# Optimization experiments

Measured on AMD Instinct MI355X. Metric: run time of the kernel, lower is better.

Reference implementation:

```python
import jax, jax.numpy as jnp
import numpy as np

N_NODES = 100000
N_REL = 5
IN_F = 128
HID = 128

def _glorot(key, shape):
    fan_in, fan_out = shape[-2], shape[-1]
    s = jnp.sqrt(6.0 / (fan_in + fan_out))
    return jax.random.uniform(key, shape, jnp.float32, -s, s)

def setup_inputs() -> dict:
    key = jax.random.key(0)
    ks = jax.random.split(key, 16)
    x = jax.random.normal(ks[0], (N_NODES, IN_F), jnp.float32)
    edge_index = jax.random.randint(ks[1], (2, 1600000), 0, N_NODES, jnp.int32)
    edge_type = jax.random.randint(ks[2], (1600000,), 0, N_REL, jnp.int32)
    d = {"x": x, "edge_index": edge_index, "edge_type": edge_type}
    dims = [(IN_F, HID), (HID, HID), (HID, HID)]
    for li, (fi, fo) in enumerate(dims, start=1):
        d[f"W{li}"] = _glorot(ks[3 * li], (N_REL, fi, fo))        # per-relation weights
        d[f"root{li}"] = _glorot(ks[3 * li + 1], (fi, fo))        # root/self weight
        d[f"b{li}"] = jnp.zeros((fo,), jnp.float32)               # bias
    return d

def _rgcn_conv(x, src, dst, edge_type, W, root, b):
    # out = x @ root + b + sum_r segment_mean_r(x[src] @ W_r -> dst)
    out = x @ root + b
    for r in range(N_REL):  # small fixed relation count
        m = (edge_type == r).astype(x.dtype)                      # [E]
        h = (x @ W[r])[src] * m[:, None]                          # [E, out]
        s = jax.ops.segment_sum(h, dst, num_segments=N_NODES)     # [N, out]
        c = jax.ops.segment_sum(m, dst, num_segments=N_NODES)     # [N]
        out = out + s / jnp.maximum(c, 1.0)[:, None]
    return out

def reference(x, edge_index, edge_type, W1, root1, b1, W2, root2, b2, W3, root3, b3):
    src, dst = edge_index[0], edge_index[1]
    # dropout is identity in eval mode; applied as identity here
    h = jax.nn.relu(_rgcn_conv(x, src, dst, edge_type, W1, root1, b1))
    h = jax.nn.relu(_rgcn_conv(h, src, dst, edge_type, W2, root2, b2))
    h = jax.nn.relu(_rgcn_conv(h, src, dst, edge_type, W3, root3, b3))
    return h
```

## Files before the change

kernel.cpp:

```cpp
#include <hip/hip_runtime.h>

#define N_NODES_C 100000
#define N_REL_C 5
#define N_TOT (N_REL_C * N_NODES_C)
#define FEAT 128
#define KTOT 768
#define BM 128
#define GBK 64

typedef __attribute__((ext_vector_type(8))) short bf16x8;
typedef __attribute__((ext_vector_type(4))) float f32x4;

__device__ inline unsigned short f2bf(float f) {
    union { float f; unsigned int u; } v; v.f = f;
    return (unsigned short)((v.u + 0x7FFFu + ((v.u >> 16) & 1u)) >> 16);
}

__device__ __forceinline__ void g2l16(const void* g, void* l) {
    __builtin_amdgcn_global_load_lds((const __attribute__((address_space(1))) unsigned int*)g,
                                     (__attribute__((address_space(3))) unsigned int*)l,
                                     16, 0, 0);
}

__global__ __launch_bounds__(256) void count_edges(const int* __restrict__ dst,
                                                   const int* __restrict__ et,
                                                   int* __restrict__ cnt, int E) {
    int e = blockIdx.x * 256 + threadIdx.x;
    if (e < E) atomicAdd(&cnt[et[e] * N_NODES_C + dst[e]], 1);
}

__global__ __launch_bounds__(256) void make_inv(const int* __restrict__ cnt,
                                                float* __restrict__ inv, int n) {
    int i = blockIdx.x * 256 + threadIdx.x;
    if (i < n) inv[i] = 1.0f / (float)(cnt[i] > 1 ? cnt[i] : 1);
}

__global__ __launch_bounds__(256) void scan_block(const int* __restrict__ cnt,
                                                  int* __restrict__ rowptr,
                                                  int* __restrict__ bsum, int n) {
    __shared__ int sh[256];
    int tid = threadIdx.x;
    int i = blockIdx.x * 256 + tid;
    int v = (i < n) ? cnt[i] : 0;
    sh[tid] = v;
    __syncthreads();
#pragma unroll
    for (int o = 1; o < 256; o <<= 1) {
        int t = (tid >= o) ? sh[tid - o] : 0;
        __syncthreads();
        sh[tid] += t;
        __syncthreads();
    }
    if (i < n) rowptr[i] = sh[tid] - v;
    if (tid == 255) bsum[blockIdx.x] = sh[255];
}

__global__ __launch_bounds__(256) void scan_bsum(int* __restrict__ bsum, int nb) {
    __shared__ int sh[256];
    __shared__ int carry;
    int tid = threadIdx.x;
    if (tid == 0) carry = 0;
    __syncthreads();
    for (int base = 0; base < nb; base += 256) {
        int i = base + tid;
        int v = (i < nb) ? bsum[i] : 0;
        sh[tid] = v;
        __syncthreads();
#pragma unroll
        for (int o = 1; o < 256; o <<= 1) {
            int t = (tid >= o) ? sh[tid - o] : 0;
            __syncthreads();
            sh[tid] += t;
            __syncthreads();
        }
        int excl = sh[tid] - v + carry;
        int chunk_total = sh[255];
        __syncthreads();
        if (i < nb) bsum[i] = excl;
        if (tid == 0) carry += chunk_total;
        __syncthreads();
    }
}

__global__ __launch_bounds__(256) void scan_add(int* __restrict__ rowptr,
                                                const int* __restrict__ bsum,
                                                int n, int Etot) {
    int i = blockIdx.x * 256 + threadIdx.x;
    if (i < n) rowptr[i] += bsum[blockIdx.x];
    if (i == 0) rowptr[n] = Etot;
}

__global__ __launch_bounds__(256) void fill_csr(const int* __restrict__ src,
                                                const int* __restrict__ dst,
                                                const int* __restrict__ et,
                                                int* __restrict__ cursor,
                                                int* __restrict__ esrc, int E) {
    int e = blockIdx.x * 256 + threadIdx.x;
    if (e < E) {
        int pos = atomicAdd(&cursor[et[e] * N_NODES_C + dst[e]], 1);
        esrc[pos] = src[e];
    }
}

__global__ __launch_bounds__(256) void convert_x(const float* __restrict__ x,
                                                 unsigned short* __restrict__ xb, int n4) {
    int i = blockIdx.x * 256 + threadIdx.x;
    if (i >= n4) return;
    float4 v = ((const float4*)x)[i];
    ushort4 o;
    o.x = f2bf(v.x); o.y = f2bf(v.y); o.z = f2bf(v.z); o.w = f2bf(v.w);
    ((ushort4*)xb)[i] = o;
}

__global__ __launch_bounds__(256) void convert_w(const float* __restrict__ root,
                                                 const float* __restrict__ W,
                                                 unsigned short* __restrict__ Bt) {
    int idx = blockIdx.x * 256 + threadIdx.x;
    if (idx >= FEAT * KTOT) return;
    int c = idx / KTOT;
    int kv = idx - c * KTOT;
    float val;
    if (kv < FEAT) {
        val = root[kv * FEAT + c];
    } else {
        int r = (kv - FEAT) >> 7;
        int kk = (kv - FEAT) & 127;
        val = W[((size_t)r * FEAT + kk) * FEAT + c];
    }
    Bt[idx] = f2bf(val);
}

__global__ __launch_bounds__(256) void gather_mean(const unsigned short* __restrict__ hb,
                                                   const int* __restrict__ esrc,
                                                   const int* __restrict__ rowptr,
                                                   const float* __restrict__ inv,
                                                   unsigned short* __restrict__ agg,
                                                   int chunk0, int CL) {
    int qw = threadIdx.x >> 4;
    int seg = threadIdx.x & 15;
    int local = blockIdx.x * 16 + qw;
    if (local >= CL) return;
    int r = blockIdx.y;
    int node = chunk0 + local;
    int lo = rowptr[r * N_NODES_C + node];
    int hi = rowptr[r * N_NODES_C + node + 1];

    float acc[8];
#pragma unroll
    for (int j = 0; j < 8; j++) acc[j] = 0.f;

    for (int e = lo; e < hi; e++) {
        int s = esrc[e];
        uint4 u = *(const uint4*)(hb + ((size_t)s << 7) + seg * 8);
        union { unsigned int u; float f; } t;
        t.u = u.x << 16;         acc[0] += t.f;
        t.u = u.x & 0xFFFF0000u; acc[1] += t.f;
        t.u = u.y << 16;         acc[2] += t.f;
        t.u = u.y & 0xFFFF0000u; acc[3] += t.f;
        t.u = u.z << 16;         acc[4] += t.f;
        t.u = u.z & 0xFFFF0000u; acc[5] += t.f;
        t.u = u.w << 16;         acc[6] += t.f;
        t.u = u.w & 0xFFFF0000u; acc[7] += t.f;
    }
    float sc = inv[r * N_NODES_C + node];
    uint4 o;
    o.x = ((unsigned int)f2bf(acc[1] * sc) << 16) | f2bf(acc[0] * sc);
    o.y = ((unsigned int)f2bf(acc[3] * sc) << 16) | f2bf(acc[2] * sc);
    o.z = ((unsigned int)f2bf(acc[5] * sc) << 16) | f2bf(acc[4] * sc);
    o.w = ((unsigned int)f2bf(acc[7] * sc) << 16) | f2bf(acc[6] * sc);
    *(uint4*)(agg + (((size_t)r * CL + local) << 7) + seg * 8) = o;
}

__global__ __launch_bounds__(256) void rgcn_gemm(const unsigned short* __restrict__ hb,
                                                 const unsigned short* __restrict__ agg,
                                                 const unsigned short* __restrict__ Bt,
                                                 const float* __restrict__ bias,
                                                 float* __restrict__ outf,
                                                 unsigned short* __restrict__ outb,
                                                 int chunk0, int CL) {
    __shared__ unsigned short As[BM * GBK];
    __shared__ unsigned short Bs[FEAT * GBK];

    const int tid = threadIdx.x;
    const int w = tid >> 6, lane = tid & 63;
    const int wr = w >> 1, wc = w & 1;
    const int lm = lane & 15, lq = lane >> 4;
    const int brow0 = blockIdx.x * BM;

    f32x4 acc[4][4];
#pragma unroll
    for (int i = 0; i < 4; i++)
#pragma unroll
        for (int j = 0; j < 4; j++) acc[i][j] = (f32x4){0.f, 0.f, 0.f, 0.f};

    size_t hboff[4];
    size_t aggoff[4];
    size_t boff[4];
    int ldsbase[4];
#pragma unroll
    for (int i = 0; i < 4; i++) {
        int cid = (w * 4 + i) * 64 + lane;
        int row = cid >> 3;
        int cs = (cid & 7) ^ (row & 7);
        int gr = brow0 + row;
        if (gr >= CL) gr = CL - 1;
        hboff[i]  = ((size_t)(chunk0 + gr) << 7) + cs * 8;
        aggoff[i] = ((size_t)gr << 7) + cs * 8;
        boff[i]   = (size_t)row * KTOT + cs * 8;
        ldsbase[i] = ((w * 4 + i) * 64) * 8;
    }

    for (int kb = 0; kb < KTOT; kb += GBK) {
        __syncthreads();
        if (kb < FEAT) {
#pragma unroll
            for (int i = 0; i < 4; i++)
                g2l16(hb + hboff[i] + kb, &As[ldsbase[i]]);
        } else {
            size_t reloff = (((size_t)((kb - FEAT) >> 7)) * CL << 7) + (size_t)((kb - FEAT) & 127);
#pragma unroll
            for (int i = 0; i < 4; i++)
                g2l16(agg + aggoff[i] + reloff, &As[ldsbase[i]]);
        }
#pragma unroll
        for (int i = 0; i < 4; i++)
            g2l16(Bt + boff[i] + kb, &Bs[ldsbase[i]]);
        __syncthreads();

#pragma unroll
        for (int h = 0; h < 2; h++) {
            bf16x8 af[4], bf[4];
#pragma unroll
            for (int t = 0; t < 4; t++) {
                int row = wr * 64 + t * 16 + lm;
                int ca = (h * 4 + lq) ^ (row & 7);
                af[t] = *(const bf16x8*)&As[row * GBK + ca * 8];
                int col = wc * 64 + t * 16 + lm;
                int cb = (h * 4 + lq) ^ (col & 7);
                bf[t] = *(const bf16x8*)&Bs[col * GBK + cb * 8];
            }
#pragma unroll
            for (int i = 0; i < 4; i++)
#pragma unroll
                for (int j = 0; j < 4; j++)
                    acc[i][j] = __builtin_amdgcn_mfma_f32_16x16x32_bf16(af[i], bf[j], acc[i][j], 0, 0, 0);
        }
    }

    float bcol[4];
#pragma unroll
    for (int j = 0; j < 4; j++) bcol[j] = bias[wc * 64 + j * 16 + lm];

#pragma unroll
    for (int i = 0; i < 4; i++) {
#pragma unroll
        for (int reg = 0; reg < 4; reg++) {
            int lr = brow0 + wr * 64 + i * 16 + lq * 4 + reg;
            if (lr < CL) {
                size_t grow = (size_t)(chunk0 + lr) << 7;
#pragma unroll
                for (int j = 0; j < 4; j++) {
                    float v = acc[i][j][reg] + bcol[j];
                    v = fmaxf(v, 0.f);
                    int col = wc * 64 + j * 16 + lm;
                    if (outf) outf[grow + col] = v;
                    else outb[grow + col] = f2bf(v);
                }
            }
        }
    }
}

extern "C" void kernel_launch(void* const* d_in, const int* in_sizes, int n_in,
                              void* d_out, int out_size, void* d_ws, size_t ws_size,
                              hipStream_t stream) {
    const float* x = (const float*)d_in[0];
    const int* ei  = (const int*)d_in[1];
    const int* et  = (const int*)d_in[2];
    const int E = in_sizes[2];
    const int* src  = ei;
    const int* dstp = ei + E;

    int CL = 25000;
    if (ws_size >= 61997056ull + 100000ull * 1280ull + 589824ull) CL = 100000;
    else if (ws_size >= 61997056ull + 50000ull * 1280ull + 589824ull) CL = 50000;
    const int NCHUNK = N_NODES_C / CL;

    char* ws = (char*)d_ws;
    float* inv             = (float*)ws;
    int*   rowptr          = (int*)(ws + 2097152);
    int*   esrc            = (int*)(ws + 4194304);
    unsigned short* xbA    = (unsigned short*)(ws + 10616832);
    unsigned short* xbB    = (unsigned short*)(ws + 36306944);
    unsigned short* agg    = (unsigned short*)(ws + 61997056);
    unsigned short* BtAll  = (unsigned short*)(ws + 61997056 + (size_t)CL * 1280ull);
    int*   cnt    = (int*)(ws + 61997056);
    int*   cursor = (int*)(ws + 61997056 + 2097152);
    int*   bsum   = (int*)(ws + 61997056 + 4194304);

    const int nscan_blocks = (N_TOT + 255) / 256;

    hipMemsetAsync(cnt, 0, (size_t)N_TOT * 4, stream);
    count_edges<<<(E + 255) / 256, 256, 0, stream>>>(dstp, et, cnt, E);
    make_inv<<<(N_TOT + 255) / 256, 256, 0, stream>>>(cnt, inv, N_TOT);
    scan_block<<<nscan_blocks, 256, 0, stream>>>(cnt, rowptr, bsum, N_TOT);
    scan_bsum<<<1, 256, 0, stream>>>(bsum, nscan_blocks);
    scan_add<<<nscan_blocks, 256, 0, stream>>>(rowptr, bsum, N_TOT, E);
    hipMemcpyAsync(cursor, rowptr, (size_t)N_TOT * 4, hipMemcpyDeviceToDevice, stream);
    fill_csr<<<(E + 255) / 256, 256, 0, stream>>>(src, dstp, et, cursor, esrc, E);

    const int n4 = N_NODES_C * FEAT / 4;
    convert_x<<<(n4 + 255) / 256, 256, 0, stream>>>(x, xbA, n4);

    const float* Wp[3] = {(const float*)d_in[3], (const float*)d_in[6], (const float*)d_in[9]};
    const float* Rp[3] = {(const float*)d_in[4], (const float*)d_in[7], (const float*)d_in[10]};
    const float* Bp[3] = {(const float*)d_in[5], (const float*)d_in[8], (const float*)d_in[11]};

    const int nw = FEAT * KTOT;
    for (int l = 0; l < 3; l++)
        convert_w<<<(nw + 255) / 256, 256, 0, stream>>>(Rp[l], Wp[l],
                                                        BtAll + (size_t)l * nw);

    const int gemm_grid = (CL + BM - 1) / BM;
    dim3 ggrid((CL + 15) / 16, N_REL_C);

    for (int l = 0; l < 3; l++) {
        const unsigned short* hin = (l == 1) ? xbB : xbA;
        unsigned short* outb = (l == 0) ? xbB : ((l == 1) ? xbA : nullptr);
        float* outf = (l == 2) ? (float*)d_out : nullptr;
        for (int c = 0; c < NCHUNK; c++) {
            gather_mean<<<ggrid, 256, 0, stream>>>(hin, esrc, rowptr, inv, agg,
                                                   c * CL, CL);
            rgcn_gemm<<<gemm_grid, 256, 0, stream>>>(hin, agg, BtAll + (size_t)l * nw,
                                                     Bp[l], outf, outb, c * CL, CL);
        }
    }
}
```

Measured before the change: 729.0 us.

## Fuse neighbor mean-gather into GEMM, aggregating per relation directly into LDS

Replaces the separate gather_mean and rgcn_gemm launches with one fused kernel per layer. Each block aggregates neighbor features for its 128 nodes, one relation at a time, writes the bf16 means straight into shared memory, and runs MFMAs against the matching weight slice. This removes the round trip of the aggregated buffer through global memory and the node chunking it required. In exchange, the gather latency is serialized with the MMA work inside each block. The grid is only about 782 blocks, and the larger shared-memory footprint may limit overlap.

After: 1.284 ms. 1.76x slower.

```diff
diff --git a/kernel.cpp b/kernel.cpp
--- a/kernel.cpp
+++ b/kernel.cpp
@@ -6,7 +6,6 @@
 #define FEAT 128
 #define KTOT 768
 #define BM 128
-#define GBK 64
 
 typedef __attribute__((ext_vector_type(8))) short bf16x8;
 typedef __attribute__((ext_vector_type(4))) float f32x4;
@@ -130,61 +129,23 @@
     Bt[idx] = f2bf(val);
 }
 
-__global__ __launch_bounds__(256) void gather_mean(const unsigned short* __restrict__ hb,
-                                                   const int* __restrict__ esrc,
-                                                   const int* __restrict__ rowptr,
-                                                   const float* __restrict__ inv,
-                                                   unsigned short* __restrict__ agg,
-                                                   int chunk0, int CL) {
-    int qw = threadIdx.x >> 4;
-    int seg = threadIdx.x & 15;
-    int local = blockIdx.x * 16 + qw;
-    if (local >= CL) return;
-    int r = blockIdx.y;
-    int node = chunk0 + local;
-    int lo = rowptr[r * N_NODES_C + node];
-    int hi = rowptr[r * N_NODES_C + node + 1];
-
-    float acc[8];
-#pragma unroll
-    for (int j = 0; j < 8; j++) acc[j] = 0.f;
-
-    for (int e = lo; e < hi; e++) {
-        int s = esrc[e];
-        uint4 u = *(const uint4*)(hb + ((size_t)s << 7) + seg * 8);
-        union { unsigned int u; float f; } t;
-        t.u = u.x << 16;         acc[0] += t.f;
-        t.u = u.x & 0xFFFF0000u; acc[1] += t.f;
-        t.u = u.y << 16;         acc[2] += t.f;
-        t.u = u.y & 0xFFFF0000u; acc[3] += t.f;
-        t.u = u.z << 16;         acc[4] += t.f;
-        t.u = u.z & 0xFFFF0000u; acc[5] += t.f;
-        t.u = u.w << 16;         acc[6] += t.f;
-        t.u = u.w & 0xFFFF0000u; acc[7] += t.f;
-    }
-    float sc = inv[r * N_NODES_C + node];
-    uint4 o;
-    o.x = ((unsigned int)f2bf(acc[1] * sc) << 16) | f2bf(acc[0] * sc);
-    o.y = ((unsigned int)f2bf(acc[3] * sc) << 16) | f2bf(acc[2] * sc);
-    o.z = ((unsigned int)f2bf(acc[5] * sc) << 16) | f2bf(acc[4] * sc);
-    o.w = ((unsigned int)f2bf(acc[7] * sc) << 16) | f2bf(acc[6] * sc);
-    *(uint4*)(agg + (((size_t)r * CL + local) << 7) + seg * 8) = o;
-}
-
-__global__ __launch_bounds__(256) void rgcn_gemm(const unsigned short* __restrict__ hb,
-                                                 const unsigned short* __restrict__ agg,
-                                                 const unsigned short* __restrict__ Bt,
-                                                 const float* __restrict__ bias,
-                                                 float* __restrict__ outf,
-                                                 unsigned short* __restrict__ outb,
-                                                 int chunk0, int CL) {
-    __shared__ unsigned short As[BM * GBK];
-    __shared__ unsigned short Bs[FEAT * GBK];
+__global__ __launch_bounds__(256, 3) void rgcn_fused(
+    const unsigned short* __restrict__ hb,
+    const unsigned short* __restrict__ Bt,
+    const float* __restrict__ bias,
+    const int* __restrict__ esrc,
+    const int* __restrict__ rowptr,
+    const float* __restrict__ inv,
+    float* __restrict__ outf,
+    unsigned short* __restrict__ outb) {
+    __shared__ unsigned short As[BM * FEAT];
+    __shared__ unsigned short Bs[FEAT * 64];
 
     const int tid = threadIdx.x;
     const int w = tid >> 6, lane = tid & 63;
     const int wr = w >> 1, wc = w & 1;
     const int lm = lane & 15, lq = lane >> 4;
+    const int qw = tid >> 4, seg = tid & 15;
     const int brow0 = blockIdx.x * BM;
 
     f32x4 acc[4][4];
@@ -193,51 +154,92 @@
 #pragma unroll
         for (int j = 0; j < 4; j++) acc[i][j] = (f32x4){0.f, 0.f, 0.f, 0.f};
 
-    size_t hboff[4];
-    size_t aggoff[4];
-    size_t boff[4];
-    int ldsbase[4];
+    size_t asrc[8]; int aldsbase[8];
+#pragma unroll
+    for (int i = 0; i < 8; i++) {
+        int cid = (w * 8 + i) * 64 + lane;
+        int row = cid >> 4, c = cid & 15;
+        int cs = (c & 8) | ((c ^ (row & 7)) & 7);
+        int gr = brow0 + row;
+        if (gr >= N_NODES_C) gr = N_NODES_C - 1;
+        asrc[i] = ((size_t)gr << 7) + cs * 8;
+        aldsbase[i] = (w * 8 + i) * 64 * 8;
+    }
+    size_t bsrc[4]; int bldsbase[4];
 #pragma unroll
     for (int i = 0; i < 4; i++) {
         int cid = (w * 4 + i) * 64 + lane;
-        int row = cid >> 3;
-        int cs = (cid & 7) ^ (row & 7);
-        int gr = brow0 + row;
-        if (gr >= CL) gr = CL - 1;
-        hboff[i]  = ((size_t)(chunk0 + gr) << 7) + cs * 8;
-        aggoff[i] = ((size_t)gr << 7) + cs * 8;
-        boff[i]   = (size_t)row * KTOT + cs * 8;
-        ldsbase[i] = ((w * 4 + i) * 64) * 8;
-    }
-
-    for (int kb = 0; kb < KTOT; kb += GBK) {
-        __syncthreads();
-        if (kb < FEAT) {
-#pragma unroll
-            for (int i = 0; i < 4; i++)
-                g2l16(hb + hboff[i] + kb, &As[ldsbase[i]]);
+        int col = cid >> 3, c = cid & 7;
+        int cs = c ^ (col & 7);
+        bsrc[i] = (size_t)col * KTOT + cs * 8;
+        bldsbase[i] = (w * 4 + i) * 64 * 8;
+    }
+
+    for (int ph = 0; ph < 6; ph++) {
+        const int kv0 = ph * FEAT;
+        __syncthreads();
+#pragma unroll
+        for (int i = 0; i < 4; i++)
+            g2l16(Bt + bsrc[i] + kv0, &Bs[bldsbase[i]]);
+        if (ph == 0) {
+#pragma unroll
+            for (int i = 0; i < 8; i++)
+                g2l16(hb + asrc[i], &As[aldsbase[i]]);
         } else {
-            size_t reloff = (((size_t)((kb - FEAT) >> 7)) * CL << 7) + (size_t)((kb - FEAT) & 127);
-#pragma unroll
-            for (int i = 0; i < 4; i++)
-                g2l16(agg + aggoff[i] + reloff, &As[ldsbase[i]]);
+            const int r = ph - 1;
+            for (int n = 0; n < 8; n++) {
+                int idx = n * 16 + qw;
+                int node = brow0 + idx;
+                float a[8] = {0.f, 0.f, 0.f, 0.f, 0.f, 0.f, 0.f, 0.f};
+                float sc = 0.f;
+                if (node < N_NODES_C) {
+                    int base = r * N_NODES_C + node;
+                    int lo = rowptr[base], hi = rowptr[base + 1];
+                    for (int e = lo; e < hi; e++) {
+                        int s = esrc[e];
+                        uint4 u = *(const uint4*)(hb + ((size_t)s << 7) + seg * 8);
+                        union { unsigned int u; float f; } t;
+                        t.u = u.x << 16;         a[0] += t.f;
+                        t.u = u.x & 0xFFFF0000u; a[1] += t.f;
+                        t.u = u.y << 16;         a[2] += t.f;
+                        t.u = u.y & 0xFFFF0000u; a[3] += t.f;
+                        t.u = u.z << 16;         a[4] += t.f;
+                        t.u = u.z & 0xFFFF0000u; a[5] += t.f;
+                        t.u = u.w << 16;         a[6] += t.f;
+                        t.u = u.w & 0xFFFF0000u; a[7] += t.f;
+                    }
+                    sc = inv[base];
+                }
+                uint4 o;
+                o.x = ((unsigned int)f2bf(a[1] * sc) << 16) | f2bf(a[0] * sc);
+                o.y = ((unsigned int)f2bf(a[3] * sc) << 16) | f2bf(a[2] * sc);
+                o.z = ((unsigned int)f2bf(a[5] * sc) << 16) | f2bf(a[4] * sc);
+                o.w = ((unsigned int)f2bf(a[7] * sc) << 16) | f2bf(a[6] * sc);
+                int cs = (seg & 8) | ((seg ^ (idx & 7)) & 7);
+                *(uint4*)&As[idx * FEAT + cs * 8] = o;
+            }
         }
-#pragma unroll
-        for (int i = 0; i < 4; i++)
-            g2l16(Bt + boff[i] + kb, &Bs[ldsbase[i]]);
-        __syncthreads();
-
-#pragma unroll
-        for (int h = 0; h < 2; h++) {
+        __syncthreads();
+
+#pragma unroll
+        for (int hh = 0; hh < 4; hh++) {
+            if (hh == 2) {
+                __syncthreads();
+#pragma unroll
+                for (int i = 0; i < 4; i++)
+                    g2l16(Bt + bsrc[i] + kv0 + 64, &Bs[bldsbase[i]]);
+                __syncthreads();
+            }
             bf16x8 af[4], bf[4];
 #pragma unroll
             for (int t = 0; t < 4; t++) {
                 int row = wr * 64 + t * 16 + lm;
-                int ca = (h * 4 + lq) ^ (row & 7);
-                af[t] = *(const bf16x8*)&As[row * GBK + ca * 8];
+                int ch = hh * 4 + lq;
+                int ca = (ch & 8) | ((ch ^ (row & 7)) & 7);
+                af[t] = *(const bf16x8*)&As[row * FEAT + ca * 8];
                 int col = wc * 64 + t * 16 + lm;
-                int cb = (h * 4 + lq) ^ (col & 7);
-                bf[t] = *(const bf16x8*)&Bs[col * GBK + cb * 8];
+                int cb = ((hh & 1) * 4 + lq) ^ (col & 7);
+                bf[t] = *(const bf16x8*)&Bs[col * 64 + cb * 8];
             }
 #pragma unroll
             for (int i = 0; i < 4; i++)
@@ -256,8 +258,8 @@
 #pragma unroll
         for (int reg = 0; reg < 4; reg++) {
             int lr = brow0 + wr * 64 + i * 16 + lq * 4 + reg;
-            if (lr < CL) {
-                size_t grow = (size_t)(chunk0 + lr) << 7;
+            if (lr < N_NODES_C) {
+                size_t grow = (size_t)lr << 7;
 #pragma unroll
                 for (int j = 0; j < 4; j++) {
                     float v = acc[i][j][reg] + bcol[j];
@@ -281,22 +283,16 @@
     const int* src  = ei;
     const int* dstp = ei + E;
 
-    int CL = 25000;
-    if (ws_size >= 61997056ull + 100000ull * 1280ull + 589824ull) CL = 100000;
-    else if (ws_size >= 61997056ull + 50000ull * 1280ull + 589824ull) CL = 50000;
-    const int NCHUNK = N_NODES_C / CL;
-
     char* ws = (char*)d_ws;
     float* inv             = (float*)ws;
     int*   rowptr          = (int*)(ws + 2097152);
     int*   esrc            = (int*)(ws + 4194304);
     unsigned short* xbA    = (unsigned short*)(ws + 10616832);
     unsigned short* xbB    = (unsigned short*)(ws + 36306944);
-    unsigned short* agg    = (unsigned short*)(ws + 61997056);
-    unsigned short* BtAll  = (unsigned short*)(ws + 61997056 + (size_t)CL * 1280ull);
-    int*   cnt    = (int*)(ws + 61997056);
-    int*   cursor = (int*)(ws + 61997056 + 2097152);
-    int*   bsum   = (int*)(ws + 61997056 + 4194304);
+    unsigned short* BtAll  = (unsigned short*)(ws + 61997056);
+    int*   cnt    = (int*)(ws + 67108864);
+    int*   cursor = (int*)(ws + 69206016);
+    int*   bsum   = (int*)(ws + 71303168);
 
     const int nscan_blocks = (N_TOT + 255) / 256;
 
@@ -321,18 +317,13 @@
         convert_w<<<(nw + 255) / 256, 256, 0, stream>>>(Rp[l], Wp[l],
                                                         BtAll + (size_t)l * nw);
 
-    const int gemm_grid = (CL + BM - 1) / BM;
-    dim3 ggrid((CL + 15) / 16, N_REL_C);
+    const int fgrid = (N_NODES_C + BM - 1) / BM;
 
     for (int l = 0; l < 3; l++) {
         const unsigned short* hin = (l == 1) ? xbB : xbA;
         unsigned short* outb = (l == 0) ? xbB : ((l == 1) ? xbA : nullptr);
         float* outf = (l == 2) ? (float*)d_out : nullptr;
-        for (int c = 0; c < NCHUNK; c++) {
-            gather_mean<<<ggrid, 256, 0, stream>>>(hin, esrc, rowptr, inv, agg,
-                                                   c * CL, CL);
-            rgcn_gemm<<<gemm_grid, 256, 0, stream>>>(hin, agg, BtAll + (size_t)l * nw,
-                                                     Bp[l], outf, outb, c * CL, CL);
-        }
-    }
-}
+        rgcn_fused<<<fgrid, 256, 0, stream>>>(hin, BtAll + (size_t)l * nw, Bp[l],
+                                              esrc, rowptr, inv, outf, outb);
+    }
+}
```

## Bucket edges by destination before CSR fill, fuse cursor copy, nontemporal agg stores

Applied to the files above, without the earlier changes.

Adds a coarse bucket sort of edges by destination range (histogram, scan, scatter into packed src/dst/type pairs). The CSR fill's atomic cursor increments and esrc writes then touch a localized address range, which should improve cache locality. The device-to-device memcpy of rowptr into cursor is folded into scan_add, and aggregation stores use nontemporal hints. In exchange it adds several extra kernel launches and an extra pass over the edges through a packed buffer.

Result: slower. 868.3 us (+19.1%).

```diff
diff --git a/kernel.cpp b/kernel.cpp
--- a/kernel.cpp
+++ b/kernel.cpp
@@ -7,9 +7,11 @@
 #define KTOT 768
 #define BM 128
 #define GBK 64
+#define NBUK 64
 
 typedef __attribute__((ext_vector_type(8))) short bf16x8;
 typedef __attribute__((ext_vector_type(4))) float f32x4;
+typedef __attribute__((ext_vector_type(4))) unsigned int u32x4;
 
 __device__ inline unsigned short f2bf(float f) {
     union { float f; unsigned int u; } v; v.f = f;
@@ -84,21 +86,72 @@
 
 __global__ __launch_bounds__(256) void scan_add(int* __restrict__ rowptr,
                                                 const int* __restrict__ bsum,
+                                                int* __restrict__ cursor,
                                                 int n, int Etot) {
     int i = blockIdx.x * 256 + threadIdx.x;
-    if (i < n) rowptr[i] += bsum[blockIdx.x];
+    if (i < n) {
+        int v = rowptr[i] + bsum[blockIdx.x];
+        rowptr[i] = v;
+        cursor[i] = v;
+    }
     if (i == 0) rowptr[n] = Etot;
 }
 
-__global__ __launch_bounds__(256) void fill_csr(const int* __restrict__ src,
-                                                const int* __restrict__ dst,
-                                                const int* __restrict__ et,
-                                                int* __restrict__ cursor,
-                                                int* __restrict__ esrc, int E) {
+__global__ __launch_bounds__(256) void bucket_hist(const int* __restrict__ dst,
+                                                   int* __restrict__ bhist, int E) {
+    __shared__ int lh[NBUK];
+    if (threadIdx.x < NBUK) lh[threadIdx.x] = 0;
+    __syncthreads();
+    for (int i = blockIdx.x * 256 + threadIdx.x; i < E; i += gridDim.x * 256)
+        atomicAdd(&lh[dst[i] >> 11], 1);
+    __syncthreads();
+    if (threadIdx.x < NBUK && lh[threadIdx.x] > 0)
+        atomicAdd(&bhist[threadIdx.x], lh[threadIdx.x]);
+}
+
+__global__ void bucket_scan(const int* __restrict__ bhist, int* __restrict__ bcursor) {
+    if (threadIdx.x == 0) {
+        int a = 0;
+        for (int i = 0; i < NBUK; i++) { bcursor[i] = a; a += bhist[i]; }
+    }
+}
+
+__global__ __launch_bounds__(256) void bucket_scatter(const int* __restrict__ src,
+                                                      const int* __restrict__ dst,
+                                                      const int* __restrict__ et,
+                                                      int* __restrict__ bcursor,
+                                                      uint2* __restrict__ packed, int E) {
+    __shared__ int lh[NBUK];
+    __shared__ int lbase[NBUK];
+    int tid = threadIdx.x;
+    int e = blockIdx.x * 256 + tid;
+    if (tid < NBUK) lh[tid] = 0;
+    __syncthreads();
+    int s = 0, key = 0, pay = 0, rank = 0;
+    bool valid = (e < E);
+    if (valid) {
+        s = src[e];
+        int d = dst[e], t = et[e];
+        key = d >> 11;
+        pay = d | (t << 20);
+        rank = atomicAdd(&lh[key], 1);
+    }
+    __syncthreads();
+    if (tid < NBUK && lh[tid] > 0) lbase[tid] = atomicAdd(&bcursor[tid], lh[tid]);
+    __syncthreads();
+    if (valid) packed[lbase[key] + rank] = (uint2){(unsigned)s, (unsigned)pay};
+}
+
+__global__ __launch_bounds__(256) void fill_csr2(const uint2* __restrict__ packed,
+                                                 int* __restrict__ cursor,
+                                                 int* __restrict__ esrc, int E) {
     int e = blockIdx.x * 256 + threadIdx.x;
     if (e < E) {
-        int pos = atomicAdd(&cursor[et[e] * N_NODES_C + dst[e]], 1);
-        esrc[pos] = src[e];
+        uint2 p = packed[e];
+        int d = p.y & 0xFFFFF;
+        int t = p.y >> 20;
+        int pos = atomicAdd(&cursor[t * N_NODES_C + d], 1);
+        esrc[pos] = p.x;
     }
 }
 
@@ -163,12 +216,12 @@
         t.u = u.w & 0xFFFF0000u; acc[7] += t.f;
     }
     float sc = inv[r * N_NODES_C + node];
-    uint4 o;
+    u32x4 o;
     o.x = ((unsigned int)f2bf(acc[1] * sc) << 16) | f2bf(acc[0] * sc);
     o.y = ((unsigned int)f2bf(acc[3] * sc) << 16) | f2bf(acc[2] * sc);
     o.z = ((unsigned int)f2bf(acc[5] * sc) << 16) | f2bf(acc[4] * sc);
     o.w = ((unsigned int)f2bf(acc[7] * sc) << 16) | f2bf(acc[6] * sc);
-    *(uint4*)(agg + (((size_t)r * CL + local) << 7) + seg * 8) = o;
+    __builtin_nontemporal_store(o, (u32x4*)(agg + (((size_t)r * CL + local) << 7) + seg * 8));
 }
 
 __global__ __launch_bounds__(256) void rgcn_gemm(const unsigned short* __restrict__ hb,
@@ -294,20 +347,27 @@
     unsigned short* xbB    = (unsigned short*)(ws + 36306944);
     unsigned short* agg    = (unsigned short*)(ws + 61997056);
     unsigned short* BtAll  = (unsigned short*)(ws + 61997056 + (size_t)CL * 1280ull);
-    int*   cnt    = (int*)(ws + 61997056);
-    int*   cursor = (int*)(ws + 61997056 + 2097152);
-    int*   bsum   = (int*)(ws + 61997056 + 4194304);
+    int*   cnt     = (int*)(ws + 61997056);
+    int*   cursor  = (int*)(ws + 61997056 + 2097152);
+    int*   bsum    = (int*)(ws + 61997056 + 4194304);
+    int*   bhist   = (int*)(ws + 61997056 + 4194304 + 16384);
+    int*   bcursor = (int*)(ws + 61997056 + 4194304 + 17408);
+    uint2* packed  = (uint2*)(ws + 61997056 + 8388608);
 
     const int nscan_blocks = (N_TOT + 255) / 256;
+    const int egrid = (E + 255) / 256;
 
     hipMemsetAsync(cnt, 0, (size_t)N_TOT * 4, stream);
-    count_edges<<<(E + 255) / 256, 256, 0, stream>>>(dstp, et, cnt, E);
+    hipMemsetAsync(bhist, 0, NBUK * 4, stream);
+    count_edges<<<egrid, 256, 0, stream>>>(dstp, et, cnt, E);
     make_inv<<<(N_TOT + 255) / 256, 256, 0, stream>>>(cnt, inv, N_TOT);
     scan_block<<<nscan_blocks, 256, 0, stream>>>(cnt, rowptr, bsum, N_TOT);
     scan_bsum<<<1, 256, 0, stream>>>(bsum, nscan_blocks);
-    scan_add<<<nscan_blocks, 256, 0, stream>>>(rowptr, bsum, N_TOT, E);
-    hipMemcpyAsync(cursor, rowptr, (size_t)N_TOT * 4, hipMemcpyDeviceToDevice, stream);
-    fill_csr<<<(E + 255) / 256, 256, 0, stream>>>(src, dstp, et, cursor, esrc, E);
+    scan_add<<<nscan_blocks, 256, 0, stream>>>(rowptr, bsum, cursor, N_TOT, E);
+    bucket_hist<<<512, 256, 0, stream>>>(dstp, bhist, E);
+    bucket_scan<<<1, 64, 0, stream>>>(bhist, bcursor);
+    bucket_scatter<<<egrid, 256, 0, stream>>>(src, dstp, et, bcursor, packed, E);
+    fill_csr2<<<egrid, 256, 0, stream>>>(packed, cursor, esrc, E);
 
     const int n4 = N_NODES_C * FEAT / 4;
     convert_x<<<(n4 + 255) / 256, 256, 0, stream>>>(x, xbA, n4);
```
